# Kernel tuning notes

Measured on AMD Instinct MI355X. Metric: run time of the kernel, lower is better.

Reference implementation:

```python
import jax, jax.numpy as jnp
import numpy as np

B, N, D = 64, 197, 768
H, E, R = 12, 8, 8


def setup_inputs() -> dict:
    key = jax.random.key(0)
    ks = jax.random.split(key, 8)
    s = 0.02
    return {
        "tokens": jax.random.normal(ks[0], (B, N, D), dtype=jnp.float32),
        "qkv_w": jax.random.normal(ks[1], (3 * D, D), dtype=jnp.float32) * s,
        "qkv_b": jax.random.normal(ks[2], (3 * D,), dtype=jnp.float32) * s,
        "proj_w": jax.random.normal(ks[3], (D, D), dtype=jnp.float32) * s,
        "proj_b": jax.random.normal(ks[4], (D,), dtype=jnp.float32) * s,
        "gate_w": jax.random.normal(ks[5], (E, D), dtype=jnp.float32) * s,
        "lora_a": jax.random.normal(ks[6], (E, D, R), dtype=jnp.float32) * s,
        "lora_b": jax.random.normal(ks[7], (E, R, 3 * D), dtype=jnp.float32) * s,
    }


def reference(tokens, qkv_w, qkv_b, proj_w, proj_b, gate_w, lora_a, lora_b):
    b, n, d = tokens.shape
    hd = d // H
    scale = hd ** (-0.5)
    # frozen qkv projection: [b, n, 3d]
    qkv = jnp.einsum("bnd,kd->bnk", tokens, qkv_w) + qkv_b
    # LoRA-MoE delta (soft router over experts)
    gates = jax.nn.softmax(jnp.einsum("bnd,ed->bne", tokens, gate_w), axis=-1)
    h = jnp.einsum("bnd,edr->bner", tokens, lora_a)  # [b,n,E,R]
    delta = jnp.einsum("bner,erk,bne->bnk", h, lora_b, gates)  # [b,n,3d]
    # adding delta before the reshape is identical to per-q/k/v addition after
    qkv = (qkv + delta).reshape(b, n, 3, H, hd).transpose(2, 0, 3, 1, 4)
    q, k, v = qkv[0], qkv[1], qkv[2]  # each [b,H,n,hd]
    attn = jax.nn.softmax(jnp.einsum("bhqd,bhkd->bhqk", q, k) * scale, axis=-1)
    out = jnp.einsum("bhqk,bhkd->bhqd", attn, v)
    out = out.transpose(0, 2, 1, 3).reshape(b, n, d)
    return jnp.einsum("bnd,kd->bnk", out, proj_w) + proj_b
```

## Files before the change

### kernel.cpp

```cpp
#include <hip/hip_runtime.h>
#include <hip/hip_bf16.h>

typedef __hip_bfloat16 BF16;
typedef __attribute__((ext_vector_type(8))) short bf16x8;
typedef __attribute__((ext_vector_type(4))) short bf16x4;
typedef __attribute__((ext_vector_type(4))) float f32x4;
typedef __attribute__((ext_vector_type(4))) int int4v;
typedef __attribute__((ext_vector_type(2))) int int2v;

#define MTOK 12608
#define D_IN 768
#define KAUG 832
#define N_QKV 2304

#define AS1 __attribute__((address_space(1)))
#define AS3 __attribute__((address_space(3)))
#define SB0() __builtin_amdgcn_sched_barrier(0)

#if __has_builtin(__builtin_amdgcn_mfma_f32_16x16x16bf16_1k)
__device__ __forceinline__ f32x4 mfma16(bf16x4 a, bf16x4 b, f32x4 c) {
  return __builtin_amdgcn_mfma_f32_16x16x16bf16_1k(a, b, c, 0, 0, 0);
}
#else
__device__ __forceinline__ f32x4 mfma16(bf16x4 a, bf16x4 b, f32x4 c) {
  f32x4 d;
  asm volatile("v_mfma_f32_16x16x16_bf16 %0, %1, %2, %3"
               : "=v"(d) : "v"(a), "v"(b), "0"(c));
  return d;
}
#endif

__global__ __launch_bounds__(256) void prep_waug_k(const float* __restrict__ qkv_w,
                                                   const float* __restrict__ lora_b,
                                                   BF16* __restrict__ Waug) {
  int idx = blockIdx.x*256 + threadIdx.x;
  if (idx >= N_QKV*KAUG) return;
  int k = idx / KAUG, c = idx - k*KAUG;
  float v = (c < D_IN) ? qkv_w[k*D_IN + c] : lora_b[(size_t)(c - D_IN)*N_QKV + k];
  Waug[idx] = (BF16)v;
}

__global__ __launch_bounds__(256) void prep_pb_k(const float* __restrict__ proj_w,
                                                 BF16* __restrict__ Pb) {
  int idx = blockIdx.x*256 + threadIdx.x;
  if (idx < D_IN*D_IN) Pb[idx] = (BF16)proj_w[idx];
}

__global__ __launch_bounds__(256) void prep_lat_k(const float* __restrict__ lora_a,
                                                  BF16* __restrict__ LAt) {
  int idx = blockIdx.x*256 + threadIdx.x;
  if (idx >= 64*D_IN) return;
  int j = idx / D_IN, d = idx - j*D_IN;
  LAt[idx] = (BF16)lora_a[(size_t)(j >> 3)*6144 + d*8 + (j & 7)];
}

__global__ __launch_bounds__(256) void token_prep_k(const float* __restrict__ tokens,
                                                    const float* __restrict__ gate_w,
                                                    BF16* __restrict__ Aaug,
                                                    float* __restrict__ gates) {
  int w = blockIdx.x*4 + (threadIdx.x >> 6);
  int lane = threadIdx.x & 63;
  if (w >= MTOK) return;
  const float* x = tokens + (size_t)w*D_IN;
  float xv[12];
  #pragma unroll
  for (int i=0;i<12;++i) xv[i] = x[lane + 64*i];
  #pragma unroll
  for (int i=0;i<12;++i) Aaug[(size_t)w*KAUG + lane + 64*i] = (BF16)xv[i];
  float g[8] = {0,0,0,0,0,0,0,0};
  #pragma unroll
  for (int i=0;i<12;++i) {
    int d = lane + 64*i;
    #pragma unroll
    for (int e=0;e<8;++e) g[e] += xv[i]*gate_w[e*D_IN + d];
  }
  #pragma unroll
  for (int e=0;e<8;++e) {
    #pragma unroll
    for (int off=32; off; off >>= 1) g[e] += __shfl_xor(g[e], off);
  }
  float mx = g[0];
  #pragma unroll
  for (int e=1;e<8;++e) mx = fmaxf(mx, g[e]);
  float pe[8]; float ssum = 0.f;
  #pragma unroll
  for (int e=0;e<8;++e) { pe[e] = __expf(g[e]-mx); ssum += pe[e]; }
  float inv = 1.f/ssum;
  if (lane < 8) {
    float val = 0.f;
    #pragma unroll
    for (int e=0;e<8;++e) val = (lane==e) ? pe[e]*inv : val;
    gates[(size_t)w*8 + lane] = val;
  }
}

template<int ROWS>
__device__ __forceinline__ void stage_bt(const BF16* __restrict__ g, int ldg, int row0, int M,
                                         BF16* lds, int kbase, int t) {
  constexpr int NIT = ROWS*8/256;
  #pragma unroll
  for (int it=0; it<NIT; ++it) {
    int c = it*256 + t;
    int r = c >> 3, kc = c & 7;
    int rg = row0 + r;
    rg = (rg < M) ? rg : (M-1);
    const BF16* gp = g + (size_t)rg*ldg + kbase + kc*8;
    BF16* lp = lds + (it*256 + (t & ~63))*8;
    __builtin_amdgcn_global_load_lds((const AS1 void*)gp, (AS3 void*)lp, 16, 0, 0);
  }
}

template<int BM, int BN, int EPI>
__global__ __launch_bounds__(256,3) void gemm_bt_k(const BF16* __restrict__ A, int lda,
                                                   const BF16* __restrict__ Bt, int ldb,
                                                   const float* __restrict__ aux,
                                                   void* __restrict__ Cv, int ldc,
                                                   int M, int K) {
  constexpr int BK = 64;
  constexpr int WM = BM/2, WN = BN/2;
  constexpr int MF = WM/16, NF = WN/16;
  __shared__ BF16 Al[BM*BK];
  __shared__ BF16 Bl[BN*BK];
  const int n0 = blockIdx.x*BN, m0 = blockIdx.y*BM;
  const int t = threadIdx.x, lane = t & 63, wid = t >> 6;
  const int wm = (wid >> 1)*WM, wn = (wid & 1)*WN;
  f32x4 acc[MF][NF] = {};
  const int KT = K/BK;
  for (int kt=0; kt<KT; ++kt) {
    stage_bt<BM>(A, lda, m0, M, Al, kt*BK, t);
    stage_bt<BN>(Bt, ldb, n0, 1<<30, Bl, kt*BK, t);
    __syncthreads();
    #pragma unroll
    for (int kk=0; kk<2; ++kk) {
      bf16x8 a[MF], b[NF];
      const int col = kk*32 + (lane >> 4)*8;
      #pragma unroll
      for (int m=0;m<MF;++m) a[m] = *(const bf16x8*)(Al + (wm + m*16 + (lane & 15))*BK + col);
      #pragma unroll
      for (int n=0;n<NF;++n) b[n] = *(const bf16x8*)(Bl + (wn + n*16 + (lane & 15))*BK + col);
      #pragma unroll
      for (int m=0;m<MF;++m)
        #pragma unroll
        for (int n=0;n<NF;++n)
          acc[m][n] = __builtin_amdgcn_mfma_f32_16x16x32_bf16(a[m], b[n], acc[m][n], 0, 0, 0);
    }
    __syncthreads();
  }
  #pragma unroll
  for (int m=0;m<MF;++m) {
    #pragma unroll
    for (int n=0;n<NF;++n) {
      const int rb = m0 + wm + m*16 + (lane >> 4)*4;
      const int c = n0 + wn + n*16 + (lane & 15);
      #pragma unroll
      for (int j=0;j<4;++j) {
        const int r = rb + j;
        if (r < M) {
          float v = acc[m][n][j];
          if (EPI == 0) {
            v *= aux[(size_t)r*8 + (c >> 3)];
            ((BF16*)Cv)[(size_t)r*ldc + c] = (BF16)v;
          } else if (EPI == 1) {
            v += aux[c];
            ((BF16*)Cv)[(size_t)r*ldc + c] = (BF16)v;
          } else {
            v += aux[c];
            ((float*)Cv)[(size_t)r*ldc + c] = v;
          }
        }
      }
    }
  }
}

template<int EPI, int NBN, int LDA, int LDB, int LDC>
__global__ __launch_bounds__(256,2) void gemm2_k(const BF16* __restrict__ A,
                                                 const BF16* __restrict__ Bt,
                                                 const float* __restrict__ bias,
                                                 void* __restrict__ Cv,
                                                 int M, int K) {
  __shared__ BF16 Lsh[2][2][8192];
  const int t = threadIdx.x, lane = t & 63, wid = t >> 6;
  const int nwg = gridDim.x;
  const int q8 = nwg >> 3, r8 = nwg & 7;
  const int xcd = blockIdx.x & 7, pos = blockIdx.x >> 3;
  const int wg = (xcd < r8 ? xcd*(q8+1) : r8*(q8+1) + (xcd - r8)*q8) + pos;
  const int mb = wg / NBN, nb = wg - mb*NBN;
  const int m0 = mb*128, n0 = nb*128;
  const int KT = K/64;
  const int q4 = lane & 15;
  const int wm = (wid >> 1)*64, wn = (wid & 1)*64;

  const BF16 *sA[4], *sB[4];
  #pragma unroll
  for (int it=0; it<4; ++it) {
    int c = it*256 + t;
    int r = c >> 3, p = c & 7;
    int sc = p ^ (r & 7);
    int ra = m0 + r; ra = ra < M ? ra : M-1;
    sA[it] = A  + (size_t)ra*LDA + sc*8;
    sB[it] = Bt + (size_t)(n0 + r)*LDB + sc*8;
  }
  auto stageAB = [&](int buf, int tile) {
    #pragma unroll
    for (int it=0; it<4; ++it)
      __builtin_amdgcn_global_load_lds((const AS1 void*)(sA[it] + tile*64),
        (AS3 void*)(&Lsh[buf][0][0] + (it*256 + (t & ~63))*8), 16, 0, 0);
    #pragma unroll
    for (int it=0; it<4; ++it)
      __builtin_amdgcn_global_load_lds((const AS1 void*)(sB[it] + tile*64),
        (AS3 void*)(&Lsh[buf][1][0] + (it*256 + (t & ~63))*8), 16, 0, 0);
  };

  const int sw = (q4 & 7) << 3;
  const int ck[2] = { (((lane >> 4)*8)) ^ sw, ((32 + (lane >> 4)*8)) ^ sw };

  f32x4 acc[4][4] = {};
  stageAB(0, 0);
  asm volatile("s_waitcnt vmcnt(0)" ::: "memory"); SB0();
  __builtin_amdgcn_s_barrier();

  for (int kt = 0; kt < KT; ++kt) {
    const int buf = kt & 1;
    if (kt+1 < KT) stageAB(buf^1, kt+1);
    bf16x8 a[4][2], b[4][2];
    #pragma unroll
    for (int m=0;m<4;++m)
      #pragma unroll
      for (int kk=0;kk<2;++kk)
        a[m][kk] = *(const bf16x8*)(&Lsh[buf][0][0] + (wm + m*16 + q4)*64 + ck[kk]);
    #pragma unroll
    for (int n=0;n<4;++n)
      #pragma unroll
      for (int kk=0;kk<2;++kk)
        b[n][kk] = *(const bf16x8*)(&Lsh[buf][1][0] + (wn + n*16 + q4)*64 + ck[kk]);
    asm volatile("s_waitcnt lgkmcnt(0)" ::: "memory"); SB0();
    __builtin_amdgcn_s_setprio(1);
    #pragma unroll
    for (int kk=0;kk<2;++kk)
      #pragma unroll
      for (int m=0;m<4;++m)
        #pragma unroll
        for (int n=0;n<4;++n)
          acc[m][n] = __builtin_amdgcn_mfma_f32_16x16x32_bf16(a[m][kk], b[n][kk], acc[m][n], 0,0,0);
    __builtin_amdgcn_s_setprio(0);
    SB0();
    if (kt+1 < KT) asm volatile("s_waitcnt vmcnt(0)" ::: "memory");
    SB0();
    __builtin_amdgcn_s_barrier();
  }

  float bv[4];
  #pragma unroll
  for (int n=0;n<4;++n) bv[n] = bias[n0 + wn + n*16 + q4];
  #pragma unroll
  for (int m=0;m<4;++m) {
    #pragma unroll
    for (int j=0;j<4;++j) {
      const int r = m0 + wm + m*16 + (lane >> 4)*4 + j;
      if (r < M) {
        #pragma unroll
        for (int n=0;n<4;++n) {
          float v = acc[m][n][j] + bv[n];
          const size_t idx = (size_t)r*LDC + n0 + wn + n*16 + q4;
          if (EPI == 1) ((BF16*)Cv)[idx] = (BF16)v;
          else          ((float*)Cv)[idx] = v;
        }
      }
    }
  }
}

__device__ __forceinline__ int pack2bf(float lo, float hi) {
  BF16 a = (BF16)lo, b = (BF16)hi;
  unsigned short al = *(unsigned short*)&a, bh = *(unsigned short*)&b;
  return (int)(((unsigned)bh << 16) | (unsigned)al);
}

__global__ __launch_bounds__(256,2) void attn_k(const BF16* __restrict__ QKV,
                                                BF16* __restrict__ O) {
  constexpr int KSTR = 72;
  constexpr int VSTR = 232;
  __shared__ BF16 Kl[208*KSTR];
  __shared__ BF16 Vt[64*VSTR];
  const int bh = blockIdx.x;
  const int b = bh / 12, h = bh - b*12;
  const size_t rowbase = (size_t)b*197;
  const int t = threadIdx.x, lane = t & 63, wid = t >> 6;
  const BF16 z = (BF16)0.0f;
  for (int c = t; c < 208*8; c += 256) {
    int r = c >> 3, kc = c & 7;
    int4v val = {0,0,0,0};
    if (r < 197) val = *(const int4v*)(QKV + (rowbase + r)*N_QKV + 768 + h*64 + kc*8);
    *(int4v*)(Kl + r*KSTR + kc*8) = val;
  }
  for (int c = t; c < 208*8; c += 256) {
    int r = c >> 3, kc = c & 7;
    if (r < 197) {
      int4v val = *(const int4v*)(QKV + (rowbase + r)*N_QKV + 1536 + h*64 + kc*8);
      const BF16* pv = (const BF16*)&val;
      #pragma unroll
      for (int i=0;i<8;++i) Vt[(kc*8 + i)*VSTR + r] = pv[i];
    } else {
      #pragma unroll
      for (int i=0;i<8;++i) Vt[(kc*8 + i)*VSTR + r] = z;
    }
  }
  __syncthreads();

  const int g = lane >> 4;
  const int q4 = lane & 15;

  for (int chunk = wid; chunk < 13; chunk += 4) {
    const int q0 = chunk*16;
    int qr = q0 + q4;
    qr = (qr < 197) ? qr : 196;
    bf16x8 qa[2];
    #pragma unroll
    for (int kk=0;kk<2;++kk)
      qa[kk] = *(const bf16x8*)(QKV + (rowbase + qr)*N_QKV + h*64 + kk*32 + g*8);
    f32x4 zf = {0.f,0.f,0.f,0.f};
    f32x4 s[13];
    #pragma unroll
    for (int nf=0;nf<13;++nf) s[nf] = zf;
    #pragma unroll
    for (int nf=0;nf<13;++nf) {
      #pragma unroll
      for (int kk=0;kk<2;++kk) {
        bf16x8 kb = *(const bf16x8*)(Kl + (nf*16 + q4)*KSTR + kk*32 + g*8);
        s[nf] = __builtin_amdgcn_mfma_f32_16x16x32_bf16(kb, qa[kk], s[nf], 0, 0, 0);
      }
    }
    float m = -1e30f;
    #pragma unroll
    for (int nf=0;nf<13;++nf) {
      #pragma unroll
      for (int j=0;j<4;++j) {
        const int kg = nf*16 + g*4 + j;
        float v = s[nf][j]*0.125f;
        v = (kg < 197) ? v : -1e30f;
        s[nf][j] = v;
        m = fmaxf(m, v);
      }
    }
    m = fmaxf(m, __shfl_xor(m, 16));
    m = fmaxf(m, __shfl_xor(m, 32));
    float lsum = 0.f;
    #pragma unroll
    for (int nf=0;nf<13;++nf) {
      #pragma unroll
      for (int j=0;j<4;++j) {
        float p = __expf(s[nf][j] - m);
        s[nf][j] = p;
        lsum += p;
      }
    }
    lsum += __shfl_xor(lsum, 16);
    lsum += __shfl_xor(lsum, 32);
    bf16x4 pa[13];
    #pragma unroll
    for (int nf=0;nf<13;++nf) {
      int2v pr;
      pr[0] = pack2bf(s[nf][0], s[nf][1]);
      pr[1] = pack2bf(s[nf][2], s[nf][3]);
      pa[nf] = *(bf16x4*)&pr;
    }
    f32x4 o[4] = {};
    #pragma unroll
    for (int nf=0; nf<13; ++nf) {
      #pragma unroll
      for (int df=0; df<4; ++df) {
        bf16x4 vb = *(const bf16x4*)(Vt + (df*16 + q4)*VSTR + nf*16 + g*4);
        o[df] = mfma16(pa[nf], vb, o[df]);
      }
    }
    float ldiv[4];
    #pragma unroll
    for (int j=0;j<4;++j) ldiv[j] = __shfl(lsum, g*4 + j);
    #pragma unroll
    for (int df=0; df<4; ++df) {
      #pragma unroll
      for (int j=0;j<4;++j) {
        const int r = q0 + g*4 + j;
        if (r < 197) {
          float val = o[df][j] / ldiv[j];
          O[(rowbase + r)*768 + h*64 + df*16 + q4] = (BF16)val;
        }
      }
    }
  }
}

extern "C" void kernel_launch(void* const* d_in, const int* in_sizes, int n_in,
                              void* d_out, int out_size, void* d_ws, size_t ws_size,
                              hipStream_t stream) {
  const float* tokens = (const float*)d_in[0];
  const float* qkv_w  = (const float*)d_in[1];
  const float* qkv_b  = (const float*)d_in[2];
  const float* proj_w = (const float*)d_in[3];
  const float* proj_b = (const float*)d_in[4];
  const float* gate_w = (const float*)d_in[5];
  const float* lora_a = (const float*)d_in[6];
  const float* lora_b = (const float*)d_in[7];

  size_t off = 0;
  auto take = [&](size_t bytes) {
    off = (off + 255) & ~(size_t)255;
    void* p = (char*)d_ws + off;
    off += bytes;
    return p;
  };
  BF16* Waug  = (BF16*)take((size_t)N_QKV*KAUG*2);
  BF16* Pb    = (BF16*)take((size_t)D_IN*D_IN*2);
  BF16* LAt   = (BF16*)take((size_t)64*D_IN*2);
  BF16* Aaug  = (BF16*)take((size_t)MTOK*KAUG*2);
  float* gates= (float*)take((size_t)MTOK*8*4);
  BF16* QKVb  = (BF16*)take((size_t)MTOK*N_QKV*2);
  BF16* Oc    = (BF16*)take((size_t)MTOK*D_IN*2);

  prep_waug_k<<<(N_QKV*KAUG + 255)/256, 256, 0, stream>>>(qkv_w, lora_b, Waug);
  prep_pb_k<<<(D_IN*D_IN + 255)/256, 256, 0, stream>>>(proj_w, Pb);
  prep_lat_k<<<(64*D_IN + 255)/256, 256, 0, stream>>>(lora_a, LAt);
  token_prep_k<<<MTOK/4, 256, 0, stream>>>(tokens, gate_w, Aaug, gates);
  gemm_bt_k<64,64,0><<<dim3(1, MTOK/64), 256, 0, stream>>>(
      Aaug, KAUG, LAt, D_IN, gates, (void*)(Aaug + 768), KAUG, MTOK, D_IN);
  gemm2_k<1, 18, KAUG, KAUG, N_QKV><<<99*18, 256, 0, stream>>>(
      Aaug, Waug, qkv_b, (void*)QKVb, MTOK, KAUG);
  attn_k<<<768, 256, 0, stream>>>(QKVb, Oc);
  gemm2_k<2, 6, D_IN, D_IN, D_IN><<<99*6, 256, 0, stream>>>(
      Oc, Pb, proj_b, d_out, MTOK, D_IN);
}
```

Baseline: 185.4 us.

## Vectorize token prep, batch K/V loads, stage attention output through LDS

```diff
diff --git a/kernel.cpp b/kernel.cpp
--- a/kernel.cpp
+++ b/kernel.cpp
@@ -61,18 +61,27 @@
   int w = blockIdx.x*4 + (threadIdx.x >> 6);
   int lane = threadIdx.x & 63;
   if (w >= MTOK) return;
-  const float* x = tokens + (size_t)w*D_IN;
-  float xv[12];
-  #pragma unroll
-  for (int i=0;i<12;++i) xv[i] = x[lane + 64*i];
-  #pragma unroll
-  for (int i=0;i<12;++i) Aaug[(size_t)w*KAUG + lane + 64*i] = (BF16)xv[i];
+  const float4* x4 = (const float4*)(tokens + (size_t)w*D_IN);
+  float4 xv[3];
+  #pragma unroll
+  for (int i=0;i<3;++i) xv[i] = x4[lane + 64*i];
+  #pragma unroll
+  for (int i=0;i<3;++i) {
+    ushort4 u;
+    BF16 b0 = (BF16)xv[i].x, b1 = (BF16)xv[i].y, b2 = (BF16)xv[i].z, b3 = (BF16)xv[i].w;
+    u.x = *(unsigned short*)&b0; u.y = *(unsigned short*)&b1;
+    u.z = *(unsigned short*)&b2; u.w = *(unsigned short*)&b3;
+    *(ushort4*)(Aaug + (size_t)w*KAUG + (lane + 64*i)*4) = u;
+  }
   float g[8] = {0,0,0,0,0,0,0,0};
   #pragma unroll
-  for (int i=0;i<12;++i) {
-    int d = lane + 64*i;
-    #pragma unroll
-    for (int e=0;e<8;++e) g[e] += xv[i]*gate_w[e*D_IN + d];
+  for (int i=0;i<3;++i) {
+    const int d4 = (lane + 64*i)*4;
+    #pragma unroll
+    for (int e=0;e<8;++e) {
+      float4 gw = *(const float4*)(gate_w + e*D_IN + d4);
+      g[e] += xv[i].x*gw.x + xv[i].y*gw.y + xv[i].z*gw.z + xv[i].w*gw.w;
+    }
   }
   #pragma unroll
   for (int e=0;e<8;++e) {
@@ -280,25 +289,36 @@
 __global__ __launch_bounds__(256,2) void attn_k(const BF16* __restrict__ QKV,
                                                 BF16* __restrict__ O) {
   constexpr int KSTR = 72;
-  constexpr int VSTR = 232;
+  constexpr int VSTR = 236;
+  constexpr int OSTR = 72;
   __shared__ BF16 Kl[208*KSTR];
   __shared__ BF16 Vt[64*VSTR];
+  __shared__ BF16 Ol[4][16*OSTR];
   const int bh = blockIdx.x;
   const int b = bh / 12, h = bh - b*12;
   const size_t rowbase = (size_t)b*197;
   const int t = threadIdx.x, lane = t & 63, wid = t >> 6;
   const BF16 z = (BF16)0.0f;
-  for (int c = t; c < 208*8; c += 256) {
+  int4v rk[7], rv[7];
+  int cc[7];
+  #pragma unroll
+  for (int it=0; it<7; ++it) {
+    int c = t + it*256; c = (c < 1663) ? c : 1663;
+    cc[it] = c;
     int r = c >> 3, kc = c & 7;
-    int4v val = {0,0,0,0};
-    if (r < 197) val = *(const int4v*)(QKV + (rowbase + r)*N_QKV + 768 + h*64 + kc*8);
-    *(int4v*)(Kl + r*KSTR + kc*8) = val;
-  }
-  for (int c = t; c < 208*8; c += 256) {
+    int rr = (r < 197) ? r : 196;
+    rk[it] = *(const int4v*)(QKV + (rowbase + rr)*N_QKV + 768  + h*64 + kc*8);
+    rv[it] = *(const int4v*)(QKV + (rowbase + rr)*N_QKV + 1536 + h*64 + kc*8);
+  }
+  #pragma unroll
+  for (int it=0; it<7; ++it) {
+    int c = cc[it];
     int r = c >> 3, kc = c & 7;
+    int4v kval = rk[it];
+    if (r >= 197) { kval[0]=0; kval[1]=0; kval[2]=0; kval[3]=0; }
+    *(int4v*)(Kl + r*KSTR + kc*8) = kval;
+    const BF16* pv = (const BF16*)&rv[it];
     if (r < 197) {
-      int4v val = *(const int4v*)(QKV + (rowbase + r)*N_QKV + 1536 + h*64 + kc*8);
-      const BF16* pv = (const BF16*)&val;
       #pragma unroll
       for (int i=0;i<8;++i) Vt[(kc*8 + i)*VSTR + r] = pv[i];
     } else {
@@ -377,16 +397,21 @@
     float ldiv[4];
     #pragma unroll
     for (int j=0;j<4;++j) ldiv[j] = __shfl(lsum, g*4 + j);
-    #pragma unroll
-    for (int df=0; df<4; ++df) {
-      #pragma unroll
-      for (int j=0;j<4;++j) {
-        const int r = q0 + g*4 + j;
-        if (r < 197) {
-          float val = o[df][j] / ldiv[j];
-          O[(rowbase + r)*768 + h*64 + df*16 + q4] = (BF16)val;
-        }
-      }
+    asm volatile("s_waitcnt lgkmcnt(0)" ::: "memory"); SB0();
+    #pragma unroll
+    for (int df=0; df<4; ++df)
+      #pragma unroll
+      for (int j=0;j<4;++j)
+        Ol[wid][(g*4 + j)*OSTR + df*16 + q4] = (BF16)(o[df][j] / ldiv[j]);
+    asm volatile("s_waitcnt lgkmcnt(0)" ::: "memory"); SB0();
+    #pragma unroll
+    for (int it=0; it<2; ++it) {
+      const int lr = (lane >> 3) + it*8;
+      const int chk = lane & 7;
+      const int r = q0 + lr;
+      int4v v = *(const int4v*)(&Ol[wid][lr*OSTR + chk*8]);
+      if (r < 197)
+        *(int4v*)(O + (rowbase + r)*768 + h*64 + chk*8) = v;
     }
   }
 }
```

Result: faster. 165.0 us (-11.0%).
